# Kernel tuning notes

Hardware: AMD Instinct MI355X
Metric: run time of the kernel (lower is better)

Reference implementation:

```python
import jax, jax.numpy as jnp
import numpy as np

EMBED_DIM = 1024
N_HEADS = 16
HEAD_DIM = EMBED_DIM // N_HEADS
MAX_REL_POS = 2  # hardcoded in the torch module


def _rel_index(length_q, length_k):
    # final_mat[i, j] = clip(i - j, -p, p) + p  with i over k-range, j over q-range
    rq = jnp.arange(length_q)[None, :]
    rk = jnp.arange(length_k)[:, None]
    dist = jnp.clip(rk - rq, -MAX_REL_POS, MAX_REL_POS) + MAX_REL_POS
    return dist  # (len_k, len_q) int; square when len_q == len_k


def setup_inputs() -> dict:
    key = jax.random.key(0)
    ks = jax.random.split(key, 16)
    B, S, E, H, D = 4, 1024, EMBED_DIM, N_HEADS, HEAD_DIM
    xavier = lambda k, shape: jax.random.uniform(
        k, shape, jnp.float32, -1.0, 1.0) * np.sqrt(6.0 / (shape[0] + shape[1]))
    return {
        "query": jax.random.normal(ks[0], (B, S, E), jnp.float32),
        "key": jax.random.normal(ks[1], (B, S, E), jnp.float32),
        "value": jax.random.normal(ks[2], (B, S, E), jnp.float32),
        "Wq": xavier(ks[3], (E, E)), "bq": jnp.zeros((E,), jnp.float32),
        "Wk": xavier(ks[4], (E, E)), "bk": jnp.zeros((E,), jnp.float32),
        "Wv": xavier(ks[5], (E, E)), "bv": jnp.zeros((E,), jnp.float32),
        "Wo": xavier(ks[6], (E, E)), "bo": jnp.zeros((E,), jnp.float32),
        "rpk_table": xavier(ks[7], (2 * MAX_REL_POS + 1, D)),
        "rpv_table": xavier(ks[8], (2 * MAX_REL_POS + 1, D)),
    }


def reference(query, key, value, Wq, bq, Wk, bk, Wv, bv, Wo, bo, rpk_table, rpv_table):
    B, S, E = query.shape
    H, D = N_HEADS, HEAD_DIM
    q = query @ Wq.T + bq
    _k = key @ Wk.T + bk      # computed but unused (faithful to source bug)
    v = value @ Wv.T + bv

    qh = q.reshape(B, S, H, D).transpose(0, 2, 1, 3)   # b h s d
    vh = v.reshape(B, S, H, D).transpose(0, 2, 1, 3)

    # NOTE: source uses query for both sides of the dot product
    dots = jnp.einsum('bhqd,bhkd->bhqk', qh, qh)

    idx = _rel_index(S, S)                              # (S, S)
    rpk = rpk_table[idx]                                # (S, S, D)
    rp_dots = jnp.einsum('bhqd,qkd->bhqk', qh, rpk)

    scale = jnp.sqrt(jnp.asarray(D, q.dtype))
    attn = jax.nn.softmax((dots + rp_dots) / scale, axis=-1)

    weight1 = jnp.einsum('bhqk,bhkd->bhqd', attn, vh)
    rpv = rpv_table[idx]                                # (S, S, D)
    weight2 = jnp.einsum('bhqk,qkd->bhqd', attn, rpv)

    out = (weight1 + weight2).transpose(0, 2, 1, 3).reshape(B, S, E)
    return out @ Wo.T + bo
```

## Files before the change

kernel.cpp:

```cpp
#include <hip/hip_runtime.h>


typedef _Float16 v8h __attribute__((ext_vector_type(8)));
typedef _Float16 v4h __attribute__((ext_vector_type(4)));
typedef float    v4f __attribute__((ext_vector_type(4)));

#define MFMA_F16(A_, B_, C_) __builtin_amdgcn_mfma_f32_16x16x32_f16(A_, B_, C_, 0, 0, 0)

__device__ __forceinline__ void async_copy16(const void* g, void* l) {
    __builtin_amdgcn_global_load_lds(
        (const __attribute__((address_space(1))) void*)g,
        (__attribute__((address_space(3))) void*)l, 16, 0, 0);
}

__global__ __launch_bounds__(256) void cvt5_kernel(
    const float* __restrict__ s0, const float* __restrict__ s1,
    const float* __restrict__ s2, const float* __restrict__ s3,
    const float* __restrict__ s4,
    _Float16* __restrict__ d0, _Float16* __restrict__ d1,
    _Float16* __restrict__ d2, _Float16* __restrict__ d3,
    _Float16* __restrict__ d4,
    int n0, int n1, int n2, int n3, int n4)
{
    const float* s; _Float16* d; int n;
    switch (blockIdx.y) {
        case 0:  s = s0; d = d0; n = n0; break;
        case 1:  s = s1; d = d1; n = n1; break;
        case 2:  s = s2; d = d2; n = n2; break;
        case 3:  s = s3; d = d3; n = n3; break;
        default: s = s4; d = d4; n = n4; break;
    }
    int i = (blockIdx.x * 256 + threadIdx.x) * 4;
    if (i >= n) return;
    float4 f = *(const float4*)(s + i);
    v4h o = { (_Float16)f.x, (_Float16)f.y, (_Float16)f.z, (_Float16)f.w };
    *(v4h*)(d + i) = o;
}

template<int TM>
__device__ __forceinline__ void gemm_core(const _Float16* __restrict__ A,
                                          const _Float16* __restrict__ W,
                                          const float* __restrict__ bias,
                                          int mode, void* __restrict__ outp,
                                          int row0, int col0)
{
    __shared__ __align__(16) _Float16 smem[2 * 128 * 64];
    _Float16* As = smem;
    _Float16* Bs = smem + 128 * 64;

    const int tid  = threadIdx.x;
    const int wave = tid >> 6, lane = tid & 63;
    const int quad = lane >> 4, n16 = lane & 15;
    const int wm = (TM == 128) ? (wave >> 1) : 0;
    const int wn = (TM == 128) ? (wave & 1) : wave;
    const int WCOLS = (TM == 128) ? 64 : 32;
    const int NJ = WCOLS / 16;
    const int rL = lane >> 3, c8 = lane & 7;
    const int lcs = c8 ^ rL;

    v4f acc[4][4] = {};

    for (int kb = 0; kb < 1024; kb += 64) {
        __syncthreads();
        #pragma unroll
        for (int p = 0; p < TM / 32; p++) {
            int rg = wave * (TM / 32) + p;
            int row = rg * 8 + rL;
            async_copy16(A + (size_t)(row0 + row) * 1024 + kb + lcs * 8, &As[rg * 512]);
        }
        #pragma unroll
        for (int p = 0; p < 4; p++) {
            int rg = wave * 4 + p;
            int row = rg * 8 + rL;
            async_copy16(W + (size_t)(col0 + row) * 1024 + kb + lcs * 8, &Bs[rg * 512]);
        }
        __syncthreads();
        #pragma unroll
        for (int ks = 0; ks < 64; ks += 32) {
            const int pc = ((ks >> 3) + quad) ^ (n16 & 7);
            v8h af[4], bf[4];
            #pragma unroll
            for (int i = 0; i < 4; i++)
                af[i] = *(const v8h*)(&As[(wm * 64 + i * 16 + n16) * 64 + pc * 8]);
            #pragma unroll
            for (int j = 0; j < NJ; j++)
                bf[j] = *(const v8h*)(&Bs[(wn * WCOLS + j * 16 + n16) * 64 + pc * 8]);
            #pragma unroll
            for (int i = 0; i < 4; i++)
                #pragma unroll
                for (int j = 0; j < NJ; j++)
                    acc[i][j] = MFMA_F16(af[i], bf[j], acc[i][j]);
        }
    }

    __syncthreads();
    char* scb = (char*)smem + wave * 8192;

    const int b     = (row0 + wm * 64) >> 10;
    const int srow0 = (row0 + wm * 64) & 1023;

    if (mode == 0) {
        _Float16* sc = (_Float16*)scb;
        #pragma unroll
        for (int i = 0; i < 4; i++)
            #pragma unroll
            for (int j = 0; j < 4; j++)
                #pragma unroll
                for (int r = 0; r < 4; r++) {
                    int rowL = i * 16 + quad * 4 + r, colL = j * 16 + n16;
                    float v = acc[i][j][r] + bias[col0 + wn * 64 + colL];
                    sc[rowL * 64 + (((colL >> 3) ^ (rowL & 7)) << 3) + (colL & 7)] = (_Float16)v;
                }
        int h = (col0 + wn * 64) >> 6;
        #pragma unroll
        for (int it = 0; it < 8; it++) {
            int rowR = it * 8 + (lane >> 3), cR = lane & 7;
            v8h val = *(const v8h*)(&sc[rowR * 64 + ((cR ^ (rowR & 7)) << 3)]);
            *(v8h*)((_Float16*)outp +
                    (((size_t)(b * 16 + h) * 1024 + srow0 + rowR) << 6) + cR * 8) = val;
        }
    } else if (mode == 1) {
        _Float16* sc = (_Float16*)scb;
        #pragma unroll
        for (int i = 0; i < 4; i++)
            #pragma unroll
            for (int j = 0; j < 4; j++) {
                int colL = j * 16 + n16;
                int c16 = i * 2 + (quad >> 1);
                v4h pk;
                #pragma unroll
                for (int r = 0; r < 4; r++)
                    pk[r] = (_Float16)(acc[i][j][r] + bias[col0 + wn * 64 + colL]);
                *(v4h*)(&sc[colL * 64 + ((c16 ^ (colL & 7)) << 3) + (quad & 1) * 4]) = pk;
            }
        #pragma unroll
        for (int it = 0; it < 8; it++) {
            int dR = it * 8 + (lane >> 3), scn = lane & 7;
            v8h val = *(const v8h*)(&sc[dR * 64 + ((scn ^ (dR & 7)) << 3)]);
            int cg = col0 + wn * 64 + dR;
            int h = cg >> 6, dl = cg & 63;
            *(v8h*)((_Float16*)outp +
                    ((size_t)((b * 16 + h) * 64 + dl) << 10) + srow0 + scn * 8) = val;
        }
    } else {
        float* sc = (float*)scb;
        #pragma unroll
        for (int i = 0; i < 4; i++)
            #pragma unroll
            for (int j = 0; j < 2; j++)
                #pragma unroll
                for (int r = 0; r < 4; r++) {
                    int rowL = i * 16 + quad * 4 + r, colL = j * 16 + n16;
                    sc[rowL * 32 + (((colL >> 2) ^ (rowL & 7)) << 2) + (colL & 3)] =
                        acc[i][j][r] + bias[col0 + wn * 32 + colL];
                }
        #pragma unroll
        for (int it = 0; it < 8; it++) {
            int rowR = it * 8 + (lane >> 3), cR = lane & 7;
            v4f val = *(const v4f*)(&sc[rowR * 32 + ((cR ^ (rowR & 7)) << 2)]);
            *(v4f*)((float*)outp + (size_t)(row0 + rowR) * 1024 + col0 + wn * 32 + cR * 4) = val;
        }
    }
}

__global__ __launch_bounds__(256) void gemm_qv_kernel(
    const _Float16* __restrict__ Aq, const _Float16* __restrict__ Av,
    const _Float16* __restrict__ Wq, const _Float16* __restrict__ Wv,
    const float* __restrict__ bq, const float* __restrict__ bv,
    _Float16* __restrict__ q_out, _Float16* __restrict__ v_out)
{
    int id = blockIdx.x;
    int y = (id & 7) | (((id >> 3) & 3) << 3);
    int x = (id >> 5) & 7;
    int z = id >> 8;
    gemm_core<128>(z ? Av : Aq, z ? Wv : Wq, z ? bv : bq, z ? 1 : 0,
                   z ? (void*)v_out : (void*)q_out, y * 128, x * 128);
}

__global__ __launch_bounds__(256) void gemm_o_kernel(
    const _Float16* __restrict__ A, const _Float16* __restrict__ W,
    const float* __restrict__ bias, float* __restrict__ outp)
{
    int id = blockIdx.x;
    int y = (id & 7) | (((id >> 3) & 7) << 3);
    int x = id >> 6;
    gemm_core<64>(A, W, bias, 2, (void*)outp, y * 64, x * 128);
}

__global__ __launch_bounds__(256) void attn_kernel(
    const _Float16* __restrict__ qb,
    const _Float16* __restrict__ vt,
    const float* __restrict__ rpk, const float* __restrict__ rpv,
    _Float16* __restrict__ attn_o)
{
    const int blk = blockIdx.x;
    const int bh = blk & 63;
    const int q0 = (blk >> 6) * 64;
    const int tid = threadIdx.x;
    const int wave = tid >> 6, lane = tid & 63;
    const int quad = lane >> 4, n16 = lane & 15;
    const int qw = q0 + wave * 16;
    const _Float16* Qh = qb + (size_t)bh * 1024 * 64;
    const _Float16* Vh = vt + (size_t)bh * 64 * 1024;

    __shared__ __align__(16) _Float16 Ks[2][64 * 64];
    __shared__ __align__(16) _Float16 Vs[2][64 * 64];
    __shared__ __align__(16) _Float16 Ps[4][16 * 64];

    const int rL = lane >> 3, c8 = lane & 7;
    const int lcs = c8 ^ rL;

    #pragma unroll
    for (int p = 0; p < 2; p++) {
        int c = wave * 2 + p;
        int row = c * 8 + rL;
        async_copy16(Qh + (size_t)row * 64 + lcs * 8, &Ks[0][c * 512]);
        async_copy16(Vh + (size_t)row * 1024 + lcs * 8, &Vs[0][c * 512]);
    }

    float* rqs_w = (float*)&Ps[wave][0];
    {
        int m = lane >> 2, seg = lane & 3;
        const _Float16* qrow = Qh + (size_t)(qw + m) * 64 + seg * 16;
        v8h qa = *(const v8h*)(qrow);
        v8h qc = *(const v8h*)(qrow + 8);
        float qd[16];
        #pragma unroll
        for (int x = 0; x < 8; x++) { qd[x] = (float)qa[x]; qd[8 + x] = (float)qc[x]; }
        float qq = 0.f;
        #pragma unroll
        for (int x = 0; x < 16; x++) qq += qd[x] * qd[x];
        qq += __shfl_xor(qq, 1);
        qq += __shfl_xor(qq, 2);
        #pragma unroll
        for (int t = 0; t < 5; t++) {
            float s = 0.f;
            #pragma unroll
            for (int x = 0; x < 16; x++) s += qd[x] * rpk[t * 64 + seg * 16 + x];
            s += __shfl_xor(s, 1);
            s += __shfl_xor(s, 2);
            if (seg == 0) rqs_w[m * 5 + t] = (s - qq) * 0.125f;
        }
    }

    v8h aq0 = *(const v8h*)(Qh + (size_t)(qw + n16) * 64 + quad * 8);
    v8h aq1 = *(const v8h*)(Qh + (size_t)(qw + n16) * 64 + 32 + quad * 8);

    __syncthreads();

    float rc[5];
    #pragma unroll
    for (int t = 0; t < 5; t++) rc[t] = rqs_w[n16 * 5 + t];

    float bkt[5] = {0.f, 0.f, 0.f, 0.f, 0.f};
    v4f O[4] = {};

    const int pphys0 = quad ^ (n16 & 7);
    const int pphys1 = (quad + 4) ^ (n16 & 7);

    for (int it = 0; it < 16; ++it) {
        const int cur = it & 1;
        const int kb = it * 64;
        if (it + 1 < 16) {
            const int nxt = 1 - cur;
            const int kn = kb + 64;
            #pragma unroll
            for (int p = 0; p < 2; p++) {
                int c = wave * 2 + p;
                int row = c * 8 + rL;
                async_copy16(Qh + (size_t)(kn + row) * 64 + lcs * 8, &Ks[nxt][c * 512]);
                async_copy16(Vh + (size_t)row * 1024 + kn + lcs * 8, &Vs[nxt][c * 512]);
            }
        }

        #pragma unroll
        for (int t = 0; t < 4; t++) {
            v8h ak0 = *(const v8h*)(&Ks[cur][(t * 16 + n16) * 64 + pphys0 * 8]);
            v8h ak1 = *(const v8h*)(&Ks[cur][(t * 16 + n16) * 64 + pphys1 * 8]);
            v4f s = {0.f, 0.f, 0.f, 0.f};
            s = MFMA_F16(ak0, aq0, s);
            s = MFMA_F16(ak1, aq1, s);
            const int dqt = qw - kb - t * 16;
            float pv[4];
            if (dqt >= 32) {
                #pragma unroll
                for (int r = 0; r < 4; r++) {
                    float p = __expf(fmaf(s[r], 0.125f, rc[4]));
                    pv[r] = p; bkt[4] += p;
                }
            } else if (dqt <= -32) {
                #pragma unroll
                for (int r = 0; r < 4; r++) {
                    float p = __expf(fmaf(s[r], 0.125f, rc[0]));
                    pv[r] = p; bkt[0] += p;
                }
            } else {
                #pragma unroll
                for (int r = 0; r < 4; r++) {
                    int diff = dqt + n16 - quad * 4 - r;
                    float rv = diff >= 2  ? rc[4]
                             : diff == 1  ? rc[3]
                             : diff == 0  ? rc[2]
                             : diff == -1 ? rc[1]
                                          : rc[0];
                    float p = __expf(fmaf(s[r], 0.125f, rv));
                    pv[r] = p;
                    bkt[4] += (diff >= 2)  ? p : 0.f;
                    bkt[3] += (diff == 1)  ? p : 0.f;
                    bkt[2] += (diff == 0)  ? p : 0.f;
                    bkt[1] += (diff == -1) ? p : 0.f;
                    bkt[0] += (diff <= -2) ? p : 0.f;
                }
            }
            v4h pk = { (_Float16)pv[0], (_Float16)pv[1], (_Float16)pv[2], (_Float16)pv[3] };
            int c16 = t * 2 + (quad >> 1);
            *(v4h*)(&Ps[wave][n16 * 64 + ((c16 ^ (n16 & 7)) << 3) + (quad & 1) * 4]) = pk;
        }

        v8h pf0 = *(const v8h*)(&Ps[wave][n16 * 64 + pphys0 * 8]);
        v8h pf1 = *(const v8h*)(&Ps[wave][n16 * 64 + pphys1 * 8]);
        #pragma unroll
        for (int dt = 0; dt < 4; dt++) {
            v8h av0 = *(const v8h*)(&Vs[cur][(dt * 16 + n16) * 64 + pphys0 * 8]);
            v8h av1 = *(const v8h*)(&Vs[cur][(dt * 16 + n16) * 64 + pphys1 * 8]);
            O[dt] = MFMA_F16(av0, pf0, O[dt]);
            O[dt] = MFMA_F16(av1, pf1, O[dt]);
        }

        __syncthreads();
    }

    #pragma unroll
    for (int t = 0; t < 5; t++) {
        bkt[t] += __shfl_xor(bkt[t], 16);
        bkt[t] += __shfl_xor(bkt[t], 32);
    }
    float l = bkt[0] + bkt[1] + bkt[2] + bkt[3] + bkt[4];
    float inv = 1.0f / l;
    int q = qw + n16;
    size_t orow = (size_t)((bh >> 4) * 1024 + q) * 1024 + (bh & 15) * 64;
    #pragma unroll
    for (int dt = 0; dt < 4; dt++) {
        int d0 = dt * 16 + quad * 4;
        v4h st;
        #pragma unroll
        for (int r = 0; r < 4; r++) {
            int d = d0 + r;
            float w2 = bkt[4] * rpv[4 * 64 + d] + bkt[3] * rpv[3 * 64 + d]
                     + bkt[2] * rpv[2 * 64 + d] + bkt[1] * rpv[1 * 64 + d]
                     + bkt[0] * rpv[0 * 64 + d];
            st[r] = (_Float16)((O[dt][r] + w2) * inv);
        }
        *(v4h*)(attn_o + orow + d0) = st;
    }
}

extern "C" void kernel_launch(void* const* d_in, const int* in_sizes, int n_in,
                              void* d_out, int out_size, void* d_ws, size_t ws_size,
                              hipStream_t stream)
{
    const float* query = (const float*)d_in[0];
    const float* value = (const float*)d_in[2];
    const float* Wq = (const float*)d_in[3];
    const float* bq = (const float*)d_in[4];
    const float* Wv = (const float*)d_in[7];
    const float* bv = (const float*)d_in[8];
    const float* Wo = (const float*)d_in[9];
    const float* bo = (const float*)d_in[10];
    const float* rpk = (const float*)d_in[11];
    const float* rpv = (const float*)d_in[12];
    float* out = (float*)d_out;

    char* ws = (char*)d_ws;
    const size_t MB = 1024 * 1024;
    _Float16* q_bhsd = (_Float16*)(ws);
    _Float16* v_t    = (_Float16*)(ws + 8 * MB);
    _Float16* q16    = (_Float16*)(ws + 16 * MB);
    _Float16* attn_o = (_Float16*)(ws + 16 * MB);
    _Float16* v16    = (_Float16*)(ws + 24 * MB);
    _Float16* wq16   = (_Float16*)(ws + 32 * MB);
    _Float16* wv16   = (_Float16*)(ws + 34 * MB);
    _Float16* wo16   = (_Float16*)(ws + 36 * MB);

    cvt5_kernel<<<dim3(4096, 5), 256, 0, stream>>>(
        query, value, Wq, Wv, Wo, q16, v16, wq16, wv16, wo16,
        4096 * 1024, 4096 * 1024, 1024 * 1024, 1024 * 1024, 1024 * 1024);

    gemm_qv_kernel<<<dim3(512), 256, 0, stream>>>(
        q16, v16, wq16, wv16, bq, bv, q_bhsd, v_t);

    attn_kernel<<<dim3(1024), 256, 0, stream>>>(q_bhsd, v_t, rpk, rpv, attn_o);

    gemm_o_kernel<<<dim3(512), 256, 0, stream>>>(attn_o, wo16, bo, out);
}
```

Measured before the change: 203.9 us.

## Keep attention probabilities in registers and retile QV GEMM to 64-row blocks

In the attention kernel, the probability tile is now packed straight into MFMA B-operand registers with cvt_pkrtz, and the V loads are permuted to match the new k ordering. This removes the per-wave LDS round trip for P and frees its shared memory. Separately, the Q/V projection GEMM switches from 128x128 to 64x128 tiles with a compile-time mode template, doubling the grid and reordering block indices. The changes trade more V loads (4x v4h instead of 2x v8h) and a round-to-zero conversion for less LDS traffic and better occupancy or wave balance in the GEMM.

Measured after the change: 205.7 us. Within noise of the previous version (+0.9%).

```diff
diff --git a/kernel.cpp b/kernel.cpp
--- a/kernel.cpp
+++ b/kernel.cpp
@@ -11,6 +11,10 @@
     __builtin_amdgcn_global_load_lds(
         (const __attribute__((address_space(1))) void*)g,
         (__attribute__((address_space(3))) void*)l, 16, 0, 0);
+}
+
+__device__ __forceinline__ v8h cat4(v4h a, v4h b) {
+    return __builtin_shufflevector(a, b, 0, 1, 2, 3, 4, 5, 6, 7);
 }
 
 __global__ __launch_bounds__(256) void cvt5_kernel(
@@ -37,28 +41,32 @@
     *(v4h*)(d + i) = o;
 }
 
-template<int TM>
+template<int TM, int MODE>
 __device__ __forceinline__ void gemm_core(const _Float16* __restrict__ A,
                                           const _Float16* __restrict__ W,
                                           const float* __restrict__ bias,
-                                          int mode, void* __restrict__ outp,
+                                          void* __restrict__ outp,
                                           int row0, int col0)
 {
-    __shared__ __align__(16) _Float16 smem[2 * 128 * 64];
+    constexpr int WCOLS = (TM == 128) ? 64 : 32;
+    constexpr int NJ = WCOLS / 16;
+    constexpr int CH = WCOLS / 8;
+    constexpr int SC_H = (MODE == 2) ? 4096 : 64 * WCOLS;
+    constexpr int STG_H = (TM + 128) * 64;
+    constexpr int TOT_H = (STG_H > 4 * SC_H) ? STG_H : 4 * SC_H;
+    __shared__ __align__(16) _Float16 smem[TOT_H];
     _Float16* As = smem;
-    _Float16* Bs = smem + 128 * 64;
+    _Float16* Bs = smem + TM * 64;
 
     const int tid  = threadIdx.x;
     const int wave = tid >> 6, lane = tid & 63;
     const int quad = lane >> 4, n16 = lane & 15;
     const int wm = (TM == 128) ? (wave >> 1) : 0;
     const int wn = (TM == 128) ? (wave & 1) : wave;
-    const int WCOLS = (TM == 128) ? 64 : 32;
-    const int NJ = WCOLS / 16;
     const int rL = lane >> 3, c8 = lane & 7;
     const int lcs = c8 ^ rL;
 
-    v4f acc[4][4] = {};
+    v4f acc[4][NJ] = {};
 
     for (int kb = 0; kb < 1024; kb += 64) {
         __syncthreads();
@@ -78,7 +86,7 @@
         #pragma unroll
         for (int ks = 0; ks < 64; ks += 32) {
             const int pc = ((ks >> 3) + quad) ^ (n16 & 7);
-            v8h af[4], bf[4];
+            v8h af[4], bf[NJ];
             #pragma unroll
             for (int i = 0; i < 4; i++)
                 af[i] = *(const v8h*)(&As[(wm * 64 + i * 16 + n16) * 64 + pc * 8]);
@@ -94,56 +102,56 @@
     }
 
     __syncthreads();
-    char* scb = (char*)smem + wave * 8192;
-
     const int b     = (row0 + wm * 64) >> 10;
     const int srow0 = (row0 + wm * 64) & 1023;
-
-    if (mode == 0) {
-        _Float16* sc = (_Float16*)scb;
+    const int C0    = col0 + wn * WCOLS;
+
+    if (MODE == 0) {
+        _Float16* sc = smem + wave * SC_H;
         #pragma unroll
         for (int i = 0; i < 4; i++)
             #pragma unroll
-            for (int j = 0; j < 4; j++)
+            for (int j = 0; j < NJ; j++)
                 #pragma unroll
                 for (int r = 0; r < 4; r++) {
                     int rowL = i * 16 + quad * 4 + r, colL = j * 16 + n16;
-                    float v = acc[i][j][r] + bias[col0 + wn * 64 + colL];
-                    sc[rowL * 64 + (((colL >> 3) ^ (rowL & 7)) << 3) + (colL & 7)] = (_Float16)v;
+                    float v = acc[i][j][r] + bias[C0 + colL];
+                    sc[rowL * WCOLS + (((colL >> 3) ^ (rowL & (CH - 1))) << 3) + (colL & 7)] =
+                        (_Float16)v;
                 }
-        int h = (col0 + wn * 64) >> 6;
-        #pragma unroll
-        for (int it = 0; it < 8; it++) {
-            int rowR = it * 8 + (lane >> 3), cR = lane & 7;
-            v8h val = *(const v8h*)(&sc[rowR * 64 + ((cR ^ (rowR & 7)) << 3)]);
+        int h = C0 >> 6, dbase = C0 & 63;
+        #pragma unroll
+        for (int it = 0; it < CH; it++) {
+            int rowR = it * (64 / CH) + (lane / CH), cR = lane & (CH - 1);
+            v8h val = *(const v8h*)(&sc[rowR * WCOLS + ((cR ^ (rowR & (CH - 1))) << 3)]);
             *(v8h*)((_Float16*)outp +
-                    (((size_t)(b * 16 + h) * 1024 + srow0 + rowR) << 6) + cR * 8) = val;
-        }
-    } else if (mode == 1) {
-        _Float16* sc = (_Float16*)scb;
+                    (((size_t)(b * 16 + h) * 1024 + srow0 + rowR) << 6) + dbase + cR * 8) = val;
+        }
+    } else if (MODE == 1) {
+        _Float16* sc = smem + wave * SC_H;
         #pragma unroll
         for (int i = 0; i < 4; i++)
             #pragma unroll
-            for (int j = 0; j < 4; j++) {
+            for (int j = 0; j < NJ; j++) {
                 int colL = j * 16 + n16;
                 int c16 = i * 2 + (quad >> 1);
                 v4h pk;
                 #pragma unroll
                 for (int r = 0; r < 4; r++)
-                    pk[r] = (_Float16)(acc[i][j][r] + bias[col0 + wn * 64 + colL]);
+                    pk[r] = (_Float16)(acc[i][j][r] + bias[C0 + colL]);
                 *(v4h*)(&sc[colL * 64 + ((c16 ^ (colL & 7)) << 3) + (quad & 1) * 4]) = pk;
             }
         #pragma unroll
-        for (int it = 0; it < 8; it++) {
+        for (int it = 0; it < CH; it++) {
             int dR = it * 8 + (lane >> 3), scn = lane & 7;
             v8h val = *(const v8h*)(&sc[dR * 64 + ((scn ^ (dR & 7)) << 3)]);
-            int cg = col0 + wn * 64 + dR;
+            int cg = C0 + dR;
             int h = cg >> 6, dl = cg & 63;
             *(v8h*)((_Float16*)outp +
                     ((size_t)((b * 16 + h) * 64 + dl) << 10) + srow0 + scn * 8) = val;
         }
     } else {
-        float* sc = (float*)scb;
+        float* sc = (float*)smem + wave * 2048;
         #pragma unroll
         for (int i = 0; i < 4; i++)
             #pragma unroll
@@ -170,11 +178,12 @@
     _Float16* __restrict__ q_out, _Float16* __restrict__ v_out)
 {
     int id = blockIdx.x;
-    int y = (id & 7) | (((id >> 3) & 3) << 3);
-    int x = (id >> 5) & 7;
-    int z = id >> 8;
-    gemm_core<128>(z ? Av : Aq, z ? Wv : Wq, z ? bv : bq, z ? 1 : 0,
-                   z ? (void*)v_out : (void*)q_out, y * 128, x * 128);
+    int k8 = id & 7;
+    int z  = k8 & 1;
+    int y  = (k8 >> 1) * 16 + ((id >> 3) & 15);
+    int x  = (id >> 7) & 7;
+    if (z) gemm_core<64, 1>(Av, Wv, bv, (void*)v_out, y * 64, x * 128);
+    else   gemm_core<64, 0>(Aq, Wq, bq, (void*)q_out, y * 64, x * 128);
 }
 
 __global__ __launch_bounds__(256) void gemm_o_kernel(
@@ -182,9 +191,9 @@
     const float* __restrict__ bias, float* __restrict__ outp)
 {
     int id = blockIdx.x;
-    int y = (id & 7) | (((id >> 3) & 7) << 3);
+    int y = (id & 7) * 8 + ((id >> 3) & 7);
     int x = id >> 6;
-    gemm_core<64>(A, W, bias, 2, (void*)outp, y * 64, x * 128);
+    gemm_core<64, 2>(A, W, bias, (void*)outp, y * 64, x * 128);
 }
 
 __global__ __launch_bounds__(256) void attn_kernel(
@@ -205,7 +214,7 @@
 
     __shared__ __align__(16) _Float16 Ks[2][64 * 64];
     __shared__ __align__(16) _Float16 Vs[2][64 * 64];
-    __shared__ __align__(16) _Float16 Ps[4][16 * 64];
+    __shared__ float rqs[4][16][5];
 
     const int rL = lane >> 3, c8 = lane & 7;
     const int lcs = c8 ^ rL;
@@ -218,7 +227,6 @@
         async_copy16(Vh + (size_t)row * 1024 + lcs * 8, &Vs[0][c * 512]);
     }
 
-    float* rqs_w = (float*)&Ps[wave][0];
     {
         int m = lane >> 2, seg = lane & 3;
         const _Float16* qrow = Qh + (size_t)(qw + m) * 64 + seg * 16;
@@ -239,7 +247,7 @@
             for (int x = 0; x < 16; x++) s += qd[x] * rpk[t * 64 + seg * 16 + x];
             s += __shfl_xor(s, 1);
             s += __shfl_xor(s, 2);
-            if (seg == 0) rqs_w[m * 5 + t] = (s - qq) * 0.125f;
+            if (seg == 0) rqs[wave][m][t] = (s - qq) * 0.125f;
         }
     }
 
@@ -250,13 +258,15 @@
 
     float rc[5];
     #pragma unroll
-    for (int t = 0; t < 5; t++) rc[t] = rqs_w[n16 * 5 + t];
+    for (int t = 0; t < 5; t++) rc[t] = rqs[wave][n16][t];
 
     float bkt[5] = {0.f, 0.f, 0.f, 0.f, 0.f};
     v4f O[4] = {};
 
     const int pphys0 = quad ^ (n16 & 7);
     const int pphys1 = (quad + 4) ^ (n16 & 7);
+    const int xk = n16 & 7;
+    const int vq = quad >> 1, vo = (quad & 1) * 4;
 
     for (int it = 0; it < 16; ++it) {
         const int cur = it & 1;
@@ -273,6 +283,7 @@
             }
         }
 
+        int pkLo[4], pkHi[4];
         #pragma unroll
         for (int t = 0; t < 4; t++) {
             v8h ak0 = *(const v8h*)(&Ks[cur][(t * 16 + n16) * 64 + pphys0 * 8]);
@@ -312,19 +323,24 @@
                     bkt[0] += (diff <= -2) ? p : 0.f;
                 }
             }
-            v4h pk = { (_Float16)pv[0], (_Float16)pv[1], (_Float16)pv[2], (_Float16)pv[3] };
-            int c16 = t * 2 + (quad >> 1);
-            *(v4h*)(&Ps[wave][n16 * 64 + ((c16 ^ (n16 & 7)) << 3) + (quad & 1) * 4]) = pk;
-        }
-
-        v8h pf0 = *(const v8h*)(&Ps[wave][n16 * 64 + pphys0 * 8]);
-        v8h pf1 = *(const v8h*)(&Ps[wave][n16 * 64 + pphys1 * 8]);
+            pkLo[t] = __builtin_bit_cast(int, __builtin_amdgcn_cvt_pkrtz(pv[0], pv[1]));
+            pkHi[t] = __builtin_bit_cast(int, __builtin_amdgcn_cvt_pkrtz(pv[2], pv[3]));
+        }
+
+        union { int d[4]; v8h v; } ub0, ub1;
+        ub0.d[0] = pkLo[0]; ub0.d[1] = pkHi[0]; ub0.d[2] = pkLo[1]; ub0.d[3] = pkHi[1];
+        ub1.d[0] = pkLo[2]; ub1.d[1] = pkHi[2]; ub1.d[2] = pkLo[3]; ub1.d[3] = pkHi[3];
+        v8h bf0 = ub0.v, bf1 = ub1.v;
+
         #pragma unroll
         for (int dt = 0; dt < 4; dt++) {
-            v8h av0 = *(const v8h*)(&Vs[cur][(dt * 16 + n16) * 64 + pphys0 * 8]);
-            v8h av1 = *(const v8h*)(&Vs[cur][(dt * 16 + n16) * 64 + pphys1 * 8]);
-            O[dt] = MFMA_F16(av0, pf0, O[dt]);
-            O[dt] = MFMA_F16(av1, pf1, O[dt]);
+            const int rowd = (dt * 16 + n16) * 64;
+            v4h a0 = *(const v4h*)(&Vs[cur][rowd + ((vq     ^ xk) << 3) + vo]);
+            v4h a1 = *(const v4h*)(&Vs[cur][rowd + (((vq+2) ^ xk) << 3) + vo]);
+            v4h a2 = *(const v4h*)(&Vs[cur][rowd + (((vq+4) ^ xk) << 3) + vo]);
+            v4h a3 = *(const v4h*)(&Vs[cur][rowd + (((vq+6) ^ xk) << 3) + vo]);
+            O[dt] = MFMA_F16(cat4(a0, a1), bf0, O[dt]);
+            O[dt] = MFMA_F16(cat4(a2, a3), bf1, O[dt]);
         }
 
         __syncthreads();
@@ -386,7 +402,7 @@
         query, value, Wq, Wv, Wo, q16, v16, wq16, wv16, wo16,
         4096 * 1024, 4096 * 1024, 1024 * 1024, 1024 * 1024, 1024 * 1024);
 
-    gemm_qv_kernel<<<dim3(512), 256, 0, stream>>>(
+    gemm_qv_kernel<<<dim3(1024), 256, 0, stream>>>(
         q16, v16, wq16, wv16, bq, bv, q_bhsd, v_t);
 
     attn_kernel<<<dim3(1024), 256, 0, stream>>>(q_bhsd, v_t, rpk, rpv, attn_o);
```
